# Performance work log

Measured on AMD Instinct MI355X. Metric: run time of the kernel, lower is better.

Reference implementation:

```python
import jax, jax.numpy as jnp
import numpy as np

D_MODEL = 1024
N_HEADS = 16
D_HEAD = 64


def setup_inputs() -> dict:
    key = jax.random.key(0)
    ks = jax.random.split(key, 5)
    B, T = 2, 2048
    scale = 1.0 / np.sqrt(D_MODEL)
    x = jax.random.normal(ks[0], (B, T, D_MODEL), dtype=jnp.float32)
    Wq = jax.random.normal(ks[1], (N_HEADS * D_HEAD, D_MODEL), dtype=jnp.float32) * scale
    Wk = jax.random.normal(ks[2], (N_HEADS * D_HEAD, D_MODEL), dtype=jnp.float32) * scale
    Wv = jax.random.normal(ks[3], (N_HEADS * D_HEAD, D_MODEL), dtype=jnp.float32) * scale
    Wo = jax.random.normal(ks[4], (D_MODEL, N_HEADS * D_HEAD), dtype=jnp.float32) * scale
    return {"x": x, "Wq": Wq, "Wk": Wk, "Wv": Wv, "Wo": Wo}


def reference(x, Wq, Wk, Wv, Wo):
    B, T, D = x.shape
    # Linear(y = x @ W.T), then split heads: [B, H, T, d]
    def split_heads(y):
        return y.reshape(B, T, N_HEADS, D_HEAD).transpose(0, 2, 1, 3)
    q = split_heads(x @ Wq.T)
    k = split_heads(x @ Wk.T)
    v = split_heads(x @ Wv.T)
    scale = D_HEAD ** -0.5
    # Materialized [B, H, T, T] scores, as in the original module
    scores = jnp.einsum('bhtd,bhTd->bhtT', q, k) * scale
    attn = jax.nn.softmax(scores, axis=-1)
    y = jnp.einsum('bhtT,bhTd->bhtd', attn, v)
    y = y.transpose(0, 2, 1, 3).reshape(B, T, N_HEADS * D_HEAD)
    return y @ Wo.T
```

## Files before the change

kernel.cpp:

```cpp
#include <hip/hip_runtime.h>
#include <hip/hip_bf16.h>

typedef __attribute__((ext_vector_type(8))) short bf16x8;
typedef __attribute__((ext_vector_type(4))) float f32x4;
typedef unsigned short u16t;

#define DEVINL static __device__ __forceinline__

DEVINL u16t f2bf(float f) {
  union { __hip_bfloat16 h; u16t u; } cv;
  cv.h = __float2bfloat16(f);
  return cv.u;
}

DEVINL unsigned cvt_pk_bf16(float a, float b) {
  unsigned r;
  asm("v_cvt_pk_bf16_f32 %0, %1, %2" : "=v"(r) : "v"(a), "v"(b));
  return r;
}

DEVINL void async16(void* lds, const void* g) {
  __builtin_amdgcn_global_load_lds((const __attribute__((address_space(1))) void*)g,
                                   (__attribute__((address_space(3))) void*)lds,
                                   16, 0, 0);
}

__global__ __launch_bounds__(256) void convert_bf16(
    const float* __restrict__ x,  const float* __restrict__ wq,
    const float* __restrict__ wk, const float* __restrict__ wv,
    const float* __restrict__ wo,
    u16t* __restrict__ xb, u16t* __restrict__ wqb, u16t* __restrict__ wkb,
    u16t* __restrict__ wvb, u16t* __restrict__ wob) {
  const int blk = blockIdx.x;
  const float* src; u16t* dst; size_t off;
  if (blk < 4096)      { src = x;  dst = xb;  off = (size_t)blk * 1024; }
  else if (blk < 5120) { src = wq; dst = wqb; off = (size_t)(blk - 4096) * 1024; }
  else if (blk < 6144) { src = wk; dst = wkb; off = (size_t)(blk - 5120) * 1024; }
  else if (blk < 7168) { src = wv; dst = wvb; off = (size_t)(blk - 6144) * 1024; }
  else                 { src = wo; dst = wob; off = (size_t)(blk - 7168) * 1024; }
  const size_t i = off + (size_t)threadIdx.x * 4;
  const float4 v = *(const float4*)&src[i];
  ushort4 r;
  r.x = f2bf(v.x); r.y = f2bf(v.y); r.z = f2bf(v.z); r.w = f2bf(v.w);
  *(ushort4*)&dst[i] = r;
}

template <int MODE, int BM>
__global__ __launch_bounds__(256) void gemm_bt(
    const u16t* __restrict__ A, const u16t* __restrict__ B,
    void* __restrict__ C0, void* __restrict__ C1, void* __restrict__ C2,
    int M, int N, int K) {
  constexpr int MI = BM / 32;
  __shared__ u16t As[2][BM * 32];
  __shared__ u16t Bs[2][128 * 32];

  const int tid = threadIdx.x;
  const int lane = tid & 63;
  const int w = tid >> 6;
  const int wm = w >> 1, wn = w & 1;
  const int quad = lane >> 4, cl = lane & 15;
  const int m0 = blockIdx.y * BM;
  const int n0 = blockIdx.x * 128;

  const int srow = lane >> 2;
  const int scol = (lane & 3) * 8;

  f32x4 acc[MI][4] = {};

  for (int k0 = 0; k0 < K; k0 += 64) {
    __syncthreads();
    #pragma unroll
    for (int p = 0; p < 2; ++p) {
      #pragma unroll
      for (int ii = 0; ii < BM / 64; ++ii) {
        const int c = w + ii * 4;
        async16(&As[p][c * 512], &A[(size_t)(m0 + c * 16 + srow) * K + k0 + p * 32 + scol]);
      }
      #pragma unroll
      for (int ii = 0; ii < 2; ++ii) {
        const int c = w + ii * 4;
        async16(&Bs[p][c * 512], &B[(size_t)(n0 + c * 16 + srow) * K + k0 + p * 32 + scol]);
      }
    }
    __syncthreads();
    #pragma unroll
    for (int p = 0; p < 2; ++p) {
      bf16x8 af[MI], bfr[4];
      #pragma unroll
      for (int i = 0; i < MI; ++i)
        af[i] = *(const bf16x8*)&As[p][(wm * (BM / 2) + i * 16 + cl) * 32 + quad * 8];
      #pragma unroll
      for (int j = 0; j < 4; ++j)
        bfr[j] = *(const bf16x8*)&Bs[p][(wn * 64 + j * 16 + cl) * 32 + quad * 8];
      #pragma unroll
      for (int i = 0; i < MI; ++i)
        #pragma unroll
        for (int j = 0; j < 4; ++j)
          acc[i][j] = __builtin_amdgcn_mfma_f32_16x16x32_bf16(af[i], bfr[j], acc[i][j], 0, 0, 0);
    }
  }

  const int nz = n0 >> 10;
  #pragma unroll
  for (int i = 0; i < MI; ++i)
    #pragma unroll
    for (int j = 0; j < 4; ++j) {
      const int mb = m0 + wm * (BM / 2) + i * 16 + quad * 4;
      const int n  = n0 + wn * 64 + j * 16 + cl;
      if (MODE == 0) {
        #pragma unroll
        for (int r = 0; r < 4; ++r)
          ((float*)C0)[(size_t)(mb + r) * N + n] = acc[i][j][r];
      } else {
        const int nw = n & 1023, h = nw >> 6, d = nw & 63;
        const int b = mb >> 11, tb = mb & 2047;
        const size_t bh = (size_t)(b * 16 + h);
        if (nz == 2) {
          ushort4 v4;
          v4.x = f2bf(acc[i][j][0]); v4.y = f2bf(acc[i][j][1]);
          v4.z = f2bf(acc[i][j][2]); v4.w = f2bf(acc[i][j][3]);
          const size_t addr = (bh << 17) +
              (size_t)(((d >> 4) * 256 + (tb >> 3)) * 128 + (d & 15) * 8 + (tb & 7));
          *(ushort4*)&((u16t*)C2)[addr] = v4;
        } else if (nz == 1) {
          const size_t basea = (bh << 17) +
              (size_t)(((tb >> 4) * 8 + (d >> 3)) * 128 + (d & 7));
          #pragma unroll
          for (int r = 0; r < 4; ++r)
            ((u16t*)C1)[basea + ((tb & 15) + r) * 8] = f2bf(acc[i][j][r]);
        } else {
          #pragma unroll
          for (int r = 0; r < 4; ++r)
            ((u16t*)C0)[(bh * 2048 + tb + r) * 64 + d] =
                f2bf(acc[i][j][r] * 0.18033688011112043f);
        }
      }
    }
}

__global__ __launch_bounds__(256, 2) void flash_attn(
    const u16t* __restrict__ Q, const u16t* __restrict__ Kt,
    const u16t* __restrict__ Vt, u16t* __restrict__ Y) {
  __shared__ u16t Ps[4 * 32 * 136];
  const int tid = threadIdx.x;
  const int lane = tid & 63;
  const int w = tid >> 6;
  const int quad = lane >> 4, cl = lane & 15;
  const int bh = blockIdx.x;
  const int q0 = blockIdx.y * 128 + w * 32;
  const u16t* Kb = Kt + ((size_t)bh << 17);
  const u16t* Vb = Vt + ((size_t)bh << 17);

  bf16x8 aq[2][2];
  #pragma unroll
  for (int h = 0; h < 2; ++h)
    #pragma unroll
    for (int ks = 0; ks < 2; ++ks)
      aq[h][ks] = *(const bf16x8*)&Q[((size_t)bh * 2048 + q0 + 16 * h + cl) * 64 + ks * 32 + quad * 8];

  bf16x8 ones8;
  #pragma unroll
  for (int i = 0; i < 8; ++i) ones8[i] = (short)0x3F80;

  f32x4 o[2][4] = {};
  f32x4 psum[2] = {};

  u16t* Pw = &Ps[w * 32 * 136];

  for (int jt = 0; jt < 16; ++jt) {
    const int j0 = jt * 128;

    bf16x8 kf[2][8];
    #pragma unroll
    for (int ks = 0; ks < 2; ++ks)
      #pragma unroll
      for (int js = 0; js < 8; ++js)
        kf[ks][js] = *(const bf16x8*)&Kb[(size_t)((((j0 >> 4) + js) * 8 + ks * 4) * 128) + lane * 8];
    __builtin_amdgcn_sched_barrier(0);

    f32x4 s0[8] = {}, s1[8] = {};
    #pragma unroll
    for (int ks = 0; ks < 2; ++ks) {
      #pragma unroll
      for (int js = 0; js < 8; ++js)
        s0[js] = __builtin_amdgcn_mfma_f32_16x16x32_bf16(kf[ks][js], aq[0][ks], s0[js], 0, 0, 0);
      #pragma unroll
      for (int js = 0; js < 8; ++js)
        s1[js] = __builtin_amdgcn_mfma_f32_16x16x32_bf16(kf[ks][js], aq[1][ks], s1[js], 0, 0, 0);
    }

    bf16x8 vf[4][4];
    #pragma unroll
    for (int ks = 0; ks < 4; ++ks)
      #pragma unroll
      for (int ds = 0; ds < 4; ++ds)
        vf[ks][ds] = *(const bf16x8*)&Vb[(size_t)((ds * 256 + (j0 >> 3) + ks * 4) * 128) + lane * 8];
    __builtin_amdgcn_sched_barrier(0);

    #pragma unroll
    for (int js = 0; js < 8; ++js) {
      uint2 pk0, pk1;
      pk0.x = cvt_pk_bf16(__builtin_exp2f(s0[js][0]), __builtin_exp2f(s0[js][1]));
      pk0.y = cvt_pk_bf16(__builtin_exp2f(s0[js][2]), __builtin_exp2f(s0[js][3]));
      *(uint2*)&Pw[cl * 136 + js * 16 + quad * 4] = pk0;
      pk1.x = cvt_pk_bf16(__builtin_exp2f(s1[js][0]), __builtin_exp2f(s1[js][1]));
      pk1.y = cvt_pk_bf16(__builtin_exp2f(s1[js][2]), __builtin_exp2f(s1[js][3]));
      *(uint2*)&Pw[(16 + cl) * 136 + js * 16 + quad * 4] = pk1;
    }

    #pragma unroll
    for (int ks = 0; ks < 4; ++ks) {
      const bf16x8 ap0 = *(const bf16x8*)&Pw[cl * 136 + ks * 32 + quad * 8];
      const bf16x8 ap1 = *(const bf16x8*)&Pw[(16 + cl) * 136 + ks * 32 + quad * 8];
      psum[0] = __builtin_amdgcn_mfma_f32_16x16x32_bf16(ap0, ones8, psum[0], 0, 0, 0);
      psum[1] = __builtin_amdgcn_mfma_f32_16x16x32_bf16(ap1, ones8, psum[1], 0, 0, 0);
      #pragma unroll
      for (int ds = 0; ds < 4; ++ds) {
        o[0][ds] = __builtin_amdgcn_mfma_f32_16x16x32_bf16(ap0, vf[ks][ds], o[0][ds], 0, 0, 0);
        o[1][ds] = __builtin_amdgcn_mfma_f32_16x16x32_bf16(ap1, vf[ks][ds], o[1][ds], 0, 0, 0);
      }
    }
  }

  const int b = bh >> 4, hd = bh & 15;
  #pragma unroll
  for (int h = 0; h < 2; ++h) {
    float inv[4];
    #pragma unroll
    for (int r = 0; r < 4; ++r) inv[r] = __builtin_amdgcn_rcpf(psum[h][r]);
    #pragma unroll
    for (int ds = 0; ds < 4; ++ds)
      #pragma unroll
      for (int r = 0; r < 4; ++r) {
        const int t = q0 + 16 * h + quad * 4 + r;
        const int d = ds * 16 + cl;
        Y[((size_t)b * 2048 + t) * 1024 + hd * 64 + d] = f2bf(o[h][ds][r] * inv[r]);
      }
  }
}

extern "C" void kernel_launch(void* const* d_in, const int* in_sizes, int n_in,
                              void* d_out, int out_size, void* d_ws, size_t ws_size,
                              hipStream_t stream) {
  (void)in_sizes; (void)n_in; (void)out_size; (void)ws_size;
  const float* x  = (const float*)d_in[0];
  const float* Wq = (const float*)d_in[1];
  const float* Wk = (const float*)d_in[2];
  const float* Wv = (const float*)d_in[3];
  const float* Wo = (const float*)d_in[4];

  char* ws = (char*)d_ws;
  const size_t MB = 1024 * 1024;
  u16t* xb  = (u16t*)(ws);
  u16t* Wqb = (u16t*)(ws + 8 * MB);
  u16t* Wkb = (u16t*)(ws + 10 * MB);
  u16t* Wvb = (u16t*)(ws + 12 * MB);
  u16t* Wob = (u16t*)(ws + 14 * MB);
  u16t* Qw  = (u16t*)(ws + 16 * MB);
  u16t* Ktw = (u16t*)(ws + 24 * MB);
  u16t* Vtw = (u16t*)(ws + 32 * MB);
  u16t* Yw  = xb;

  convert_bf16<<<8192, 256, 0, stream>>>(x, Wq, Wk, Wv, Wo, xb, Wqb, Wkb, Wvb, Wob);
  gemm_bt<1, 128><<<dim3(24, 32), 256, 0, stream>>>(
      xb, Wqb, Qw, Ktw, Vtw, 4096, 3072, 1024);
  flash_attn<<<dim3(32, 16), 256, 0, stream>>>(Qw, Ktw, Vtw, Yw);
  gemm_bt<0, 64><<<dim3(8, 64), 256, 0, stream>>>(
      Yw, Wob, d_out, d_out, d_out, 4096, 1024, 1024);
}
```

Before: 191.9 us.

## Double-buffer GEMM K-loop to overlap async LDS loads with MFMA compute

Restructures the projection GEMM main loop from 'load a 64-wide K chunk, barrier, compute' into a ping-pong pipeline over 32-wide K halves. The next half is issued to the other LDS buffer before the current half is computed. This hides global-to-LDS load latency behind MFMA work and keeps the barrier count per 64 K about the same. The gain depends on the barrier waiting for outstanding loads, which caps overlap to one stage.

```diff
diff --git a/kernel.cpp b/kernel.cpp
--- a/kernel.cpp
+++ b/kernel.cpp
@@ -67,38 +67,51 @@
 
   f32x4 acc[MI][4] = {};
 
-  for (int k0 = 0; k0 < K; k0 += 64) {
+  #define STAGEP(b, kp)                                                       \
+    {                                                                         \
+      _Pragma("unroll")                                                       \
+      for (int ii = 0; ii < BM / 64; ++ii) {                                  \
+        const int c = w + ii * 4;                                             \
+        async16(&As[b][c * 512],                                              \
+                &A[(size_t)(m0 + c * 16 + srow) * K + (kp) * 32 + scol]);     \
+      }                                                                       \
+      _Pragma("unroll")                                                       \
+      for (int ii = 0; ii < 2; ++ii) {                                        \
+        const int c = w + ii * 4;                                             \
+        async16(&Bs[b][c * 512],                                              \
+                &B[(size_t)(n0 + c * 16 + srow) * K + (kp) * 32 + scol]);     \
+      }                                                                       \
+    }
+
+  #define COMPUTEP(b)                                                         \
+    {                                                                         \
+      bf16x8 af[MI], bfr[4];                                                  \
+      _Pragma("unroll")                                                       \
+      for (int i = 0; i < MI; ++i)                                            \
+        af[i] = *(const bf16x8*)&As[b][(wm * (BM / 2) + i * 16 + cl) * 32 + quad * 8]; \
+      _Pragma("unroll")                                                       \
+      for (int j = 0; j < 4; ++j)                                             \
+        bfr[j] = *(const bf16x8*)&Bs[b][(wn * 64 + j * 16 + cl) * 32 + quad * 8]; \
+      _Pragma("unroll")                                                       \
+      for (int i = 0; i < MI; ++i)                                            \
+        _Pragma("unroll")                                                     \
+        for (int j = 0; j < 4; ++j)                                           \
+          acc[i][j] = __builtin_amdgcn_mfma_f32_16x16x32_bf16(af[i], bfr[j], acc[i][j], 0, 0, 0); \
+    }
+
+  const int NP = K >> 5;
+  STAGEP(0, 0);
+  __syncthreads();
+  for (int kp = 0; kp < NP; kp += 2) {
+    if (kp + 1 < NP) STAGEP(1, kp + 1);
+    COMPUTEP(0);
     __syncthreads();
-    #pragma unroll
-    for (int p = 0; p < 2; ++p) {
-      #pragma unroll
-      for (int ii = 0; ii < BM / 64; ++ii) {
-        const int c = w + ii * 4;
-        async16(&As[p][c * 512], &A[(size_t)(m0 + c * 16 + srow) * K + k0 + p * 32 + scol]);
-      }
-      #pragma unroll
-      for (int ii = 0; ii < 2; ++ii) {
-        const int c = w + ii * 4;
-        async16(&Bs[p][c * 512], &B[(size_t)(n0 + c * 16 + srow) * K + k0 + p * 32 + scol]);
-      }
-    }
+    if (kp + 2 < NP) STAGEP(0, kp + 2);
+    COMPUTEP(1);
     __syncthreads();
-    #pragma unroll
-    for (int p = 0; p < 2; ++p) {
-      bf16x8 af[MI], bfr[4];
-      #pragma unroll
-      for (int i = 0; i < MI; ++i)
-        af[i] = *(const bf16x8*)&As[p][(wm * (BM / 2) + i * 16 + cl) * 32 + quad * 8];
-      #pragma unroll
-      for (int j = 0; j < 4; ++j)
-        bfr[j] = *(const bf16x8*)&Bs[p][(wn * 64 + j * 16 + cl) * 32 + quad * 8];
-      #pragma unroll
-      for (int i = 0; i < MI; ++i)
-        #pragma unroll
-        for (int j = 0; j < 4; ++j)
-          acc[i][j] = __builtin_amdgcn_mfma_f32_16x16x32_bf16(af[i], bfr[j], acc[i][j], 0, 0, 0);
-    }
   }
+  #undef STAGEP
+  #undef COMPUTEP
 
   const int nz = n0 >> 10;
   #pragma unroll
```

Result: no change. 191.8 us (-0.1%).
